# Optimization experiments

Hardware: AMD Instinct MI355X
Metric: run time of the kernel (lower is better)

## Reference

```python
import jax, jax.numpy as jnp
import numpy as np


def xnorm(x, g):
    # x * gamma / ||x||_2 along last dim (no eps, matching torch.norm)
    n = jnp.sqrt(jnp.sum(x * x, axis=-1, keepdims=True))
    return x * g / n


def setup_inputs() -> dict:
    key = jax.random.key(0)
    ks = jax.random.split(key, 6)
    B, N, D = 8, 8192, 512
    H, DK, DV = 8, 64, 64
    std = 0.001
    return {
        "queries": jax.random.normal(ks[0], (B, N, D), dtype=jnp.float32),
        # weights stored [in, out] (transposed vs torch Linear)
        "Wq": jax.random.normal(ks[1], (D, H * DK), dtype=jnp.float32) * std,
        "bq": jnp.zeros((H * DK,), dtype=jnp.float32),
        "Wk": jax.random.normal(ks[2], (D, H * DK), dtype=jnp.float32) * std,
        "bk": jnp.zeros((H * DK,), dtype=jnp.float32),
        "Wv": jax.random.normal(ks[3], (D, H * DV), dtype=jnp.float32) * std,
        "bv": jnp.zeros((H * DV,), dtype=jnp.float32),
        "Wo": jax.random.normal(ks[4], (H * DV, D), dtype=jnp.float32) * std,
        "bo": jnp.zeros((D,), dtype=jnp.float32),
        "gamma": jax.random.normal(ks[5], (1, H, 1, 1), dtype=jnp.float32),
    }


def reference(queries, Wq, bq, Wk, bk, Wv, bv, Wo, bo, gamma):
    B, N, D = queries.shape
    H, DK = 8, 64
    DV = 64
    q = (queries @ Wq + bq).reshape(B, N, H, DK)  # bnhd
    k = (queries @ Wk + bk).reshape(B, N, H, DK)
    v = (queries @ Wv + bv).reshape(B, N, H, DV)
    # kv = k^T @ v per (batch, head): [B,H,DK,DV]
    kv = jnp.einsum("bnhk,bnhv->bhkv", k, v)
    kv_n = xnorm(kv, gamma)                       # norm over DV axis
    q_n = xnorm(q.transpose(0, 2, 1, 3), gamma)   # bhnd, norm over DK axis
    out = jnp.einsum("bhnk,bhkv->bnhv", q_n, kv_n).reshape(B, N, H * DV)
    return out @ Wo + bo
```

## Files before the change

### kernel.cpp

```cpp
#include <hip/hip_runtime.h>

typedef __attribute__((ext_vector_type(8))) short s8v;
typedef __attribute__((ext_vector_type(4))) short s4v;
typedef __attribute__((ext_vector_type(4))) float f4v;

__device__ __forceinline__ unsigned short f2bf(float f) {
  unsigned int u = __float_as_uint(f);
  u += 0x7FFFu + ((u >> 16) & 1u);
  return (unsigned short)(u >> 16);
}
__device__ __forceinline__ float bf2f(unsigned short s) {
  return __uint_as_float(((unsigned int)s) << 16);
}

__device__ __forceinline__ void gld16(const void* g, void* l) {
  __builtin_amdgcn_global_load_lds(
      (const __attribute__((address_space(1))) unsigned int*)g,
      (__attribute__((address_space(3))) unsigned int*)l, 16, 0, 0);
}

#define TILE_SYNC() asm volatile("s_waitcnt vmcnt(0) lgkmcnt(0)\n\ts_barrier" ::: "memory")

__global__ __launch_bounds__(256)
void convert_x_kernel(const float* __restrict__ X, unsigned short* __restrict__ Xbf)
{
  size_t base = ((size_t)blockIdx.x * 256 + threadIdx.x) * 8;
  float4 a = *(const float4*)&X[base];
  float4 b = *(const float4*)&X[base + 4];
  s8v p = (s8v){ (short)f2bf(a.x), (short)f2bf(a.y), (short)f2bf(a.z), (short)f2bf(a.w),
                 (short)f2bf(b.x), (short)f2bf(b.y), (short)f2bf(b.z), (short)f2bf(b.w) };
  *(s8v*)&Xbf[base] = p;
}

__global__ __launch_bounds__(256)
void transpose_w_kernel(const float* __restrict__ Wq, const float* __restrict__ Wk,
                        const float* __restrict__ Wv, unsigned short* __restrict__ Wt)
{
  __shared__ float T[64][68];
  const int kt = blockIdx.x, nt = blockIdx.y;
  const float* W = (nt < 8) ? Wq : (nt < 16 ? Wk : Wv);
  const int n0 = (nt & 7) * 64, k0 = kt * 64;
  const int t = threadIdx.x;
  #pragma unroll
  for (int it = 0; it < 4; ++it) {
    int idx = it * 256 + t;
    int k = idx >> 4, n4 = (idx & 15) << 2;
    *(float4*)&T[k][n4] = *(const float4*)&W[(size_t)(k0 + k) * 512 + n0 + n4];
  }
  __syncthreads();
  #pragma unroll
  for (int it = 0; it < 2; ++it) {
    int idx = it * 256 + t;
    int n = idx >> 3, k8 = (idx & 7) << 3;
    s8v p;
    #pragma unroll
    for (int j = 0; j < 8; ++j) p[j] = (short)f2bf(T[k8 + j][n]);
    *(s8v*)&Wt[((size_t)nt * 64 + n) * 512 + k0 + k8] = p;
  }
}

__global__ __launch_bounds__(512, 2)
void gemm_qkv_kernel(const unsigned short* __restrict__ Xbf,
                     const unsigned short* __restrict__ Wt,
                     const float* __restrict__ bq, const float* __restrict__ bk,
                     const float* __restrict__ bv,
                     const float* __restrict__ gamma,
                     unsigned short* __restrict__ qkv)
{
  __shared__ short As[2][16384];
  __shared__ short Bs[2][16384];
  const int t = threadIdx.x;
  const int o = blockIdx.x;
  const int swz = (o & 7) * 192 + (o >> 3);
  const int nb = swz % 6, rb = swz / 6;
  const int wave = t >> 6, lane = t & 63;
  const int wm = wave & 1, wn = wave >> 1;
  const int quad = lane >> 4, l16 = lane & 15;
  const int row0 = rb * 256, ncol0 = nb * 256;

  const unsigned short* ap[4];
  const unsigned short* bp[4];
  int ldst[4];
  #pragma unroll
  for (int i = 0; i < 4; ++i) {
    int s = i * 512 + t;
    int m = s >> 3, kb = (s & 7) ^ (m & 7);
    ap[i] = Xbf + (size_t)(row0 + m) * 512 + kb * 8;
    bp[i] = Wt + (size_t)(ncol0 + m) * 512 + kb * 8;
    ldst[i] = s * 8;
  }

  f4v acc[8][4];
  #pragma unroll
  for (int i = 0; i < 8; ++i)
    #pragma unroll
    for (int j = 0; j < 4; ++j) acc[i][j] = (f4v){0.f, 0.f, 0.f, 0.f};

  #pragma unroll
  for (int i = 0; i < 4; ++i) {
    gld16(ap[i], &As[0][ldst[i]]);
    gld16(bp[i], &Bs[0][ldst[i]]);
  }
  TILE_SYNC();

  for (int kt = 0; kt < 8; ++kt) {
    const int cur = kt & 1;
    const short* Ac = As[cur];
    const short* Bc = Bs[cur];
    short* An = (short*)As[cur ^ 1];
    short* Bn = (short*)Bs[cur ^ 1];
    const int koff = (kt + 1) * 64;
    const bool pf = kt < 7;
    s8v afr[4][2], bfr[4][2];

    if (pf) {
      gld16(ap[0] + koff, &An[ldst[0]]);
      gld16(ap[1] + koff, &An[ldst[1]]);
      gld16(bp[0] + koff, &Bn[ldst[0]]);
      gld16(bp[1] + koff, &Bn[ldst[1]]);
    }
    #pragma unroll
    for (int nj = 0; nj < 4; ++nj)
      #pragma unroll
      for (int ks = 0; ks < 2; ++ks) {
        int r = wn * 64 + nj * 16 + l16;
        bfr[nj][ks] = *(const s8v*)&Bc[(r * 8 + ((ks * 4 + quad) ^ (r & 7))) * 8];
      }
    #pragma unroll
    for (int mi = 0; mi < 4; ++mi)
      #pragma unroll
      for (int ks = 0; ks < 2; ++ks) {
        int r = wm * 128 + mi * 16 + l16;
        afr[mi][ks] = *(const s8v*)&Ac[(r * 8 + ((ks * 4 + quad) ^ (r & 7))) * 8];
      }
    __builtin_amdgcn_s_setprio(1);
    #pragma unroll
    for (int mi = 0; mi < 4; ++mi)
      #pragma unroll
      for (int nj = 0; nj < 2; ++nj)
        #pragma unroll
        for (int ks = 0; ks < 2; ++ks)
          acc[mi][nj] = __builtin_amdgcn_mfma_f32_16x16x32_bf16(afr[mi][ks], bfr[nj][ks], acc[mi][nj], 0, 0, 0);
    __builtin_amdgcn_s_setprio(0);
    __builtin_amdgcn_s_barrier();

    if (pf) {
      gld16(ap[2] + koff, &An[ldst[2]]);
      gld16(ap[3] + koff, &An[ldst[3]]);
      gld16(bp[2] + koff, &Bn[ldst[2]]);
      gld16(bp[3] + koff, &Bn[ldst[3]]);
    }
    __builtin_amdgcn_s_setprio(1);
    #pragma unroll
    for (int mi = 0; mi < 4; ++mi)
      #pragma unroll
      for (int nj = 2; nj < 4; ++nj)
        #pragma unroll
        for (int ks = 0; ks < 2; ++ks)
          acc[mi][nj] = __builtin_amdgcn_mfma_f32_16x16x32_bf16(afr[mi][ks], bfr[nj][ks], acc[mi][nj], 0, 0, 0);
    __builtin_amdgcn_s_setprio(0);
    __builtin_amdgcn_s_barrier();

    #pragma unroll
    for (int mi = 0; mi < 4; ++mi)
      #pragma unroll
      for (int ks = 0; ks < 2; ++ks) {
        int r = wm * 128 + (4 + mi) * 16 + l16;
        afr[mi][ks] = *(const s8v*)&Ac[(r * 8 + ((ks * 4 + quad) ^ (r & 7))) * 8];
      }
    __builtin_amdgcn_s_setprio(1);
    #pragma unroll
    for (int mi = 0; mi < 4; ++mi)
      #pragma unroll
      for (int nj = 0; nj < 2; ++nj)
        #pragma unroll
        for (int ks = 0; ks < 2; ++ks)
          acc[4 + mi][nj] = __builtin_amdgcn_mfma_f32_16x16x32_bf16(afr[mi][ks], bfr[nj][ks], acc[4 + mi][nj], 0, 0, 0);
    __builtin_amdgcn_s_setprio(0);
    __builtin_amdgcn_s_barrier();

    __builtin_amdgcn_s_setprio(1);
    #pragma unroll
    for (int mi = 0; mi < 4; ++mi)
      #pragma unroll
      for (int nj = 2; nj < 4; ++nj)
        #pragma unroll
        for (int ks = 0; ks < 2; ++ks)
          acc[4 + mi][nj] = __builtin_amdgcn_mfma_f32_16x16x32_bf16(afr[mi][ks], bfr[nj][ks], acc[4 + mi][nj], 0, 0, 0);
    __builtin_amdgcn_s_setprio(0);
    TILE_SYNC();
  }

  #pragma unroll
  for (int nj = 0; nj < 4; ++nj) {
    int colg = ncol0 + wn * 64 + nj * 16 + l16;
    float bias;
    if (colg < 512) bias = bq[colg];
    else if (colg < 1024) bias = bk[colg - 512];
    else bias = bv[colg - 1024];
    #pragma unroll
    for (int mi = 0; mi < 8; ++mi) {
      acc[mi][nj][0] += bias; acc[mi][nj][1] += bias;
      acc[mi][nj][2] += bias; acc[mi][nj][3] += bias;
    }
  }

  if (nb < 2) {
    float g = gamma[nb * 4 + wn];
    #pragma unroll
    for (int mi = 0; mi < 8; ++mi)
      #pragma unroll
      for (int rr = 0; rr < 4; ++rr) {
        float ss = acc[mi][0][rr] * acc[mi][0][rr] + acc[mi][1][rr] * acc[mi][1][rr]
                 + acc[mi][2][rr] * acc[mi][2][rr] + acc[mi][3][rr] * acc[mi][3][rr];
        ss += __shfl_xor(ss, 1);
        ss += __shfl_xor(ss, 2);
        ss += __shfl_xor(ss, 4);
        ss += __shfl_xor(ss, 8);
        float scale = g * rsqrtf(ss);
        acc[mi][0][rr] *= scale; acc[mi][1][rr] *= scale;
        acc[mi][2][rr] *= scale; acc[mi][3][rr] *= scale;
      }
  }

  const int colbase = ncol0 + wn * 64;
  #pragma unroll
  for (int mi = 0; mi < 8; ++mi)
    #pragma unroll
    for (int nj = 0; nj < 4; ++nj)
      #pragma unroll
      for (int rr = 0; rr < 4; ++rr) {
        int row = row0 + wm * 128 + mi * 16 + quad * 4 + rr;
        int col = colbase + nj * 16 + l16;
        qkv[(size_t)row * 1536 + col] = f2bf(acc[mi][nj][rr]);
      }
}

__global__ __launch_bounds__(256)
void kv_accum_kernel(const unsigned short* __restrict__ qkv, float* __restrict__ kvpart)
{
  __shared__ float ksf[16][64];
  __shared__ float vsf[16][64];
  const int t = threadIdx.x;
  const int bh = blockIdx.x, chunk = blockIdx.y;
  const int b = bh >> 3, h = bh & 7;
  const int base_row = b * 8192 + chunk * 512;
  const int lane = t & 63, wave = t >> 6;
  const int dk0 = (lane & 7) * 8, dv0 = (lane >> 3) * 8;
  const int half = t >> 7, tt = t & 127;
  const int sr = tt >> 3, u = tt & 7;
  const int col = (half ? 1024 : 512) + h * 64 + u * 8;
  const unsigned short* src = qkv + (size_t)(base_row + sr) * 1536 + col;
  float* dstlds = half ? &vsf[sr][u * 8] : &ksf[sr][u * 8];
  float acc[8][8] = {};

  for (int it = 0; it < 32; ++it) {
    __syncthreads();
    union { int4 v; unsigned short s[8]; } raw;
    raw.v = *(const int4*)(src + (size_t)it * 16 * 1536);
    float4 lo = { bf2f(raw.s[0]), bf2f(raw.s[1]), bf2f(raw.s[2]), bf2f(raw.s[3]) };
    float4 hi = { bf2f(raw.s[4]), bf2f(raw.s[5]), bf2f(raw.s[6]), bf2f(raw.s[7]) };
    *(float4*)dstlds = lo;
    *(float4*)(dstlds + 4) = hi;
    __syncthreads();
    #pragma unroll
    for (int rr = 0; rr < 4; ++rr) {
      int r = rr * 4 + wave;
      float4 ka = *(const float4*)&ksf[r][dk0];
      float4 kb = *(const float4*)&ksf[r][dk0 + 4];
      float4 va = *(const float4*)&vsf[r][dv0];
      float4 vb = *(const float4*)&vsf[r][dv0 + 4];
      float kf[8] = { ka.x, ka.y, ka.z, ka.w, kb.x, kb.y, kb.z, kb.w };
      float vf[8] = { va.x, va.y, va.z, va.w, vb.x, vb.y, vb.z, vb.w };
      #pragma unroll
      for (int i = 0; i < 8; ++i)
        #pragma unroll
        for (int j = 0; j < 8; ++j)
          acc[i][j] = fmaf(kf[i], vf[j], acc[i][j]);
    }
  }
  float* dst = kvpart + ((size_t)(chunk * 4 + wave) * 64 + bh) * 4096;
  #pragma unroll
  for (int i = 0; i < 8; ++i) {
    *(float4*)&dst[(dk0 + i) * 64 + dv0]     = (float4){ acc[i][0], acc[i][1], acc[i][2], acc[i][3] };
    *(float4*)&dst[(dk0 + i) * 64 + dv0 + 4] = (float4){ acc[i][4], acc[i][5], acc[i][6], acc[i][7] };
  }
}

__global__ __launch_bounds__(256)
void kv_reduce_kernel(const float* __restrict__ kvpart, float* __restrict__ kvbuf)
{
  const int bh = blockIdx.x, seg = blockIdx.y, t = threadIdx.x;
  #pragma unroll
  for (int e = 0; e < 2; ++e) {
    int i = seg * 512 + e * 256 + t;
    float s = 0.f;
    for (int c = 0; c < 64; ++c) s += kvpart[((size_t)c * 64 + bh) * 4096 + i];
    kvbuf[(size_t)bh * 4096 + i] = s;
  }
}

__global__ __launch_bounds__(256)
void build_w2t_kernel(const float* __restrict__ kvbuf, const float* __restrict__ Wo,
                      const float* __restrict__ gamma, unsigned short* __restrict__ W2t)
{
  __shared__ float WoS[512][16];
  const int b = blockIdx.x, dt = blockIdx.y;
  const int d0 = dt * 16;
  const int t = threadIdx.x;
  for (int i = 0; i < 32; ++i) {
    int flat = i * 256 + t;
    int rr_ = flat >> 4, c = flat & 15;
    WoS[rr_][c] = Wo[(size_t)rr_ * 512 + d0 + c];
  }
  __syncthreads();
  for (int rr = 0; rr < 2; ++rr) {
    int r = rr * 256 + t;
    int h = r >> 6, k = r & 63;
    const float* krow = kvbuf + ((size_t)b * 8 + h) * 4096 + (size_t)k * 64;
    float ss = 0.f;
    #pragma unroll
    for (int v = 0; v < 64; v += 4) {
      float4 x = *(const float4*)&krow[v];
      ss += x.x * x.x + x.y * x.y + x.z * x.z + x.w * x.w;
    }
    float scale = gamma[h] * rsqrtf(ss);
    f4v accv[4];
    #pragma unroll
    for (int j = 0; j < 4; ++j) accv[j] = (f4v){0.f, 0.f, 0.f, 0.f};
    for (int v = 0; v < 64; ++v) {
      float m = krow[v] * scale;
      const float* w = &WoS[h * 64 + v][0];
      #pragma unroll
      for (int j4 = 0; j4 < 4; ++j4) {
        float4 ww = *(const float4*)&w[j4 * 4];
        accv[j4][0] = fmaf(m, ww.x, accv[j4][0]);
        accv[j4][1] = fmaf(m, ww.y, accv[j4][1]);
        accv[j4][2] = fmaf(m, ww.z, accv[j4][2]);
        accv[j4][3] = fmaf(m, ww.w, accv[j4][3]);
      }
    }
    #pragma unroll
    for (int j = 0; j < 16; ++j)
      W2t[((size_t)b * 512 + d0 + j) * 512 + r] = f2bf(accv[j >> 2][j & 3]);
  }
}

__global__ __launch_bounds__(512, 2)
void gemm_out_kernel(const unsigned short* __restrict__ qkv,
                     const unsigned short* __restrict__ W2t,
                     const float* __restrict__ bo,
                     float* __restrict__ out)
{
  __shared__ short As[2][16384];
  __shared__ short Bs[2][16384];
  const int t = threadIdx.x;
  const int o = blockIdx.x;
  const int swz = (o & 7) * 64 + (o >> 3);
  const int nb = swz & 1, rb = swz >> 1;
  const int wave = t >> 6, lane = t & 63;
  const int wm = wave & 1, wn = wave >> 1;
  const int quad = lane >> 4, l16 = lane & 15;
  const int row0 = rb * 256, ncol0 = nb * 256;
  const unsigned short* Wb = W2t + (size_t)(rb >> 5) * 262144;

  const unsigned short* ap[4];
  const unsigned short* bp[4];
  int ldst[4];
  #pragma unroll
  for (int i = 0; i < 4; ++i) {
    int s = i * 512 + t;
    int m = s >> 3, kb = (s & 7) ^ (m & 7);
    ap[i] = qkv + (size_t)(row0 + m) * 1536 + kb * 8;
    bp[i] = Wb + (size_t)(ncol0 + m) * 512 + kb * 8;
    ldst[i] = s * 8;
  }

  f4v acc[8][4];
  #pragma unroll
  for (int i = 0; i < 8; ++i)
    #pragma unroll
    for (int j = 0; j < 4; ++j) acc[i][j] = (f4v){0.f, 0.f, 0.f, 0.f};

  #pragma unroll
  for (int i = 0; i < 4; ++i) {
    gld16(ap[i], &As[0][ldst[i]]);
    gld16(bp[i], &Bs[0][ldst[i]]);
  }
  TILE_SYNC();

  for (int kt = 0; kt < 8; ++kt) {
    const int cur = kt & 1;
    const short* Ac = As[cur];
    const short* Bc = Bs[cur];
    short* An = (short*)As[cur ^ 1];
    short* Bn = (short*)Bs[cur ^ 1];
    const int koff = (kt + 1) * 64;
    const bool pf = kt < 7;
    s8v afr[4][2], bfr[4][2];

    if (pf) {
      gld16(ap[0] + koff, &An[ldst[0]]);
      gld16(ap[1] + koff, &An[ldst[1]]);
      gld16(bp[0] + koff, &Bn[ldst[0]]);
      gld16(bp[1] + koff, &Bn[ldst[1]]);
    }
    #pragma unroll
    for (int nj = 0; nj < 4; ++nj)
      #pragma unroll
      for (int ks = 0; ks < 2; ++ks) {
        int r = wn * 64 + nj * 16 + l16;
        bfr[nj][ks] = *(const s8v*)&Bc[(r * 8 + ((ks * 4 + quad) ^ (r & 7))) * 8];
      }
    #pragma unroll
    for (int mi = 0; mi < 4; ++mi)
      #pragma unroll
      for (int ks = 0; ks < 2; ++ks) {
        int r = wm * 128 + mi * 16 + l16;
        afr[mi][ks] = *(const s8v*)&Ac[(r * 8 + ((ks * 4 + quad) ^ (r & 7))) * 8];
      }
    __builtin_amdgcn_s_setprio(1);
    #pragma unroll
    for (int mi = 0; mi < 4; ++mi)
      #pragma unroll
      for (int nj = 0; nj < 2; ++nj)
        #pragma unroll
        for (int ks = 0; ks < 2; ++ks)
          acc[mi][nj] = __builtin_amdgcn_mfma_f32_16x16x32_bf16(afr[mi][ks], bfr[nj][ks], acc[mi][nj], 0, 0, 0);
    __builtin_amdgcn_s_setprio(0);
    __builtin_amdgcn_s_barrier();

    if (pf) {
      gld16(ap[2] + koff, &An[ldst[2]]);
      gld16(ap[3] + koff, &An[ldst[3]]);
      gld16(bp[2] + koff, &Bn[ldst[2]]);
      gld16(bp[3] + koff, &Bn[ldst[3]]);
    }
    __builtin_amdgcn_s_setprio(1);
    #pragma unroll
    for (int mi = 0; mi < 4; ++mi)
      #pragma unroll
      for (int nj = 2; nj < 4; ++nj)
        #pragma unroll
        for (int ks = 0; ks < 2; ++ks)
          acc[mi][nj] = __builtin_amdgcn_mfma_f32_16x16x32_bf16(afr[mi][ks], bfr[nj][ks], acc[mi][nj], 0, 0, 0);
    __builtin_amdgcn_s_setprio(0);
    __builtin_amdgcn_s_barrier();

    #pragma unroll
    for (int mi = 0; mi < 4; ++mi)
      #pragma unroll
      for (int ks = 0; ks < 2; ++ks) {
        int r = wm * 128 + (4 + mi) * 16 + l16;
        afr[mi][ks] = *(const s8v*)&Ac[(r * 8 + ((ks * 4 + quad) ^ (r & 7))) * 8];
      }
    __builtin_amdgcn_s_setprio(1);
    #pragma unroll
    for (int mi = 0; mi < 4; ++mi)
      #pragma unroll
      for (int nj = 0; nj < 2; ++nj)
        #pragma unroll
        for (int ks = 0; ks < 2; ++ks)
          acc[4 + mi][nj] = __builtin_amdgcn_mfma_f32_16x16x32_bf16(afr[mi][ks], bfr[nj][ks], acc[4 + mi][nj], 0, 0, 0);
    __builtin_amdgcn_s_setprio(0);
    __builtin_amdgcn_s_barrier();

    __builtin_amdgcn_s_setprio(1);
    #pragma unroll
    for (int mi = 0; mi < 4; ++mi)
      #pragma unroll
      for (int nj = 2; nj < 4; ++nj)
        #pragma unroll
        for (int ks = 0; ks < 2; ++ks)
          acc[4 + mi][nj] = __builtin_amdgcn_mfma_f32_16x16x32_bf16(afr[mi][ks], bfr[nj][ks], acc[4 + mi][nj], 0, 0, 0);
    __builtin_amdgcn_s_setprio(0);
    TILE_SYNC();
  }

  const int colbase = ncol0 + wn * 64;
  #pragma unroll
  for (int nj = 0; nj < 4; ++nj) {
    float bias = bo[colbase + nj * 16 + l16];
    #pragma unroll
    for (int mi = 0; mi < 8; ++mi)
      #pragma unroll
      for (int rr = 0; rr < 4; ++rr) {
        int row = row0 + wm * 128 + mi * 16 + quad * 4 + rr;
        int col = colbase + nj * 16 + l16;
        out[(size_t)row * 512 + col] = acc[mi][nj][rr] + bias;
      }
  }
}

extern "C" void kernel_launch(void* const* d_in, const int* in_sizes, int n_in,
                              void* d_out, int out_size, void* d_ws, size_t ws_size,
                              hipStream_t stream)
{
  (void)in_sizes; (void)n_in; (void)out_size; (void)ws_size;
  const float* X     = (const float*)d_in[0];
  const float* Wq    = (const float*)d_in[1];
  const float* bq    = (const float*)d_in[2];
  const float* Wk    = (const float*)d_in[3];
  const float* bk    = (const float*)d_in[4];
  const float* Wv    = (const float*)d_in[5];
  const float* bv    = (const float*)d_in[6];
  const float* Wo    = (const float*)d_in[7];
  const float* bo    = (const float*)d_in[8];
  const float* gamma = (const float*)d_in[9];

  char* ws = (char*)d_ws;
  unsigned short* qkv = (unsigned short*)ws;
  unsigned short* Xbf = (unsigned short*)(ws + 201326592);
  float* kvpart = (float*)(ws + 201326592);
  unsigned short* Wt  = (unsigned short*)(ws + 201326592 + 67108864);
  float* kvbuf        = (float*)(ws + 201326592 + 67108864 + 1572864);
  unsigned short* W2t = (unsigned short*)(ws + 201326592 + 67108864 + 1572864 + 1048576);

  dim3 blk(256);
  convert_x_kernel<<<16384, blk, 0, stream>>>(X, Xbf);
  transpose_w_kernel<<<dim3(8, 24), blk, 0, stream>>>(Wq, Wk, Wv, Wt);
  gemm_qkv_kernel<<<1536, dim3(512), 0, stream>>>(Xbf, Wt, bq, bk, bv, gamma, qkv);
  kv_accum_kernel<<<dim3(64, 16), blk, 0, stream>>>(qkv, kvpart);
  kv_reduce_kernel<<<dim3(64, 8), blk, 0, stream>>>(kvpart, kvbuf);
  build_w2t_kernel<<<dim3(8, 32), blk, 0, stream>>>(kvbuf, Wo, gamma, W2t);
  gemm_out_kernel<<<512, dim3(512), 0, stream>>>(qkv, W2t, bo, (float*)d_out);
}
```

Baseline: 530.6 us.

## Store K/V transposed from QKV GEMM and use MFMA for KV accumulation

The QKV GEMM now writes normalized Q into a compact row-major buffer and writes K and V transposed (feature-major along the sequence), so the KV accumulation can load MFMA operands directly from global memory and use bf16 matrix cores instead of scalar FMAs through LDS. The GEMM tile is shrunk from 256x256 with 512 threads, double-buffered and prioritized, to a 128x128 single-buffered loop with 256 threads. This removes the scalar FP32 outer-product cost in kv_accum and the strided reads of the wide qkv buffer. In exchange it gives up the software pipelining in the main GEMM and adds scattered transposed stores.

Result: faster. 504.8 us (-4.9%).

```diff
diff --git a/kernel.cpp b/kernel.cpp
--- a/kernel.cpp
+++ b/kernel.cpp
@@ -1,7 +1,6 @@
 #include <hip/hip_runtime.h>
 
 typedef __attribute__((ext_vector_type(8))) short s8v;
-typedef __attribute__((ext_vector_type(4))) short s4v;
 typedef __attribute__((ext_vector_type(4))) float f4v;
 
 __device__ __forceinline__ unsigned short f2bf(float f) {
@@ -59,156 +58,88 @@
   }
 }
 
-__global__ __launch_bounds__(512, 2)
+__global__ __launch_bounds__(256, 2)
 void gemm_qkv_kernel(const unsigned short* __restrict__ Xbf,
                      const unsigned short* __restrict__ Wt,
                      const float* __restrict__ bq, const float* __restrict__ bk,
                      const float* __restrict__ bv,
                      const float* __restrict__ gamma,
-                     unsigned short* __restrict__ qkv)
-{
-  __shared__ short As[2][16384];
-  __shared__ short Bs[2][16384];
+                     unsigned short* __restrict__ qhat,
+                     unsigned short* __restrict__ kvT)
+{
+  __shared__ short As[8192];
+  __shared__ short Bs[8192];
   const int t = threadIdx.x;
-  const int o = blockIdx.x;
-  const int swz = (o & 7) * 192 + (o >> 3);
-  const int nb = swz % 6, rb = swz / 6;
+  const int nb = blockIdx.x, rb = blockIdx.y;
   const int wave = t >> 6, lane = t & 63;
   const int wm = wave & 1, wn = wave >> 1;
   const int quad = lane >> 4, l16 = lane & 15;
-  const int row0 = rb * 256, ncol0 = nb * 256;
+  const int row0 = rb * 128;
+  const int ncol0 = nb * 128;
 
   const unsigned short* ap[4];
   const unsigned short* bp[4];
-  int ldst[4];
   #pragma unroll
   for (int i = 0; i < 4; ++i) {
-    int s = i * 512 + t;
-    int m = s >> 3, kb = (s & 7) ^ (m & 7);
+    int s = i * 256 + t;
+    int m = s >> 3;
+    int kb = (s & 7) ^ (m & 7);
     ap[i] = Xbf + (size_t)(row0 + m) * 512 + kb * 8;
     bp[i] = Wt + (size_t)(ncol0 + m) * 512 + kb * 8;
-    ldst[i] = s * 8;
-  }
-
-  f4v acc[8][4];
-  #pragma unroll
-  for (int i = 0; i < 8; ++i)
+  }
+
+  f4v acc[4][4];
+  #pragma unroll
+  for (int i = 0; i < 4; ++i)
     #pragma unroll
     for (int j = 0; j < 4; ++j) acc[i][j] = (f4v){0.f, 0.f, 0.f, 0.f};
 
-  #pragma unroll
-  for (int i = 0; i < 4; ++i) {
-    gld16(ap[i], &As[0][ldst[i]]);
-    gld16(bp[i], &Bs[0][ldst[i]]);
-  }
-  TILE_SYNC();
-
-  for (int kt = 0; kt < 8; ++kt) {
-    const int cur = kt & 1;
-    const short* Ac = As[cur];
-    const short* Bc = Bs[cur];
-    short* An = (short*)As[cur ^ 1];
-    short* Bn = (short*)Bs[cur ^ 1];
-    const int koff = (kt + 1) * 64;
-    const bool pf = kt < 7;
-    s8v afr[4][2], bfr[4][2];
-
-    if (pf) {
-      gld16(ap[0] + koff, &An[ldst[0]]);
-      gld16(ap[1] + koff, &An[ldst[1]]);
-      gld16(bp[0] + koff, &Bn[ldst[0]]);
-      gld16(bp[1] + koff, &Bn[ldst[1]]);
-    }
-    #pragma unroll
-    for (int nj = 0; nj < 4; ++nj)
-      #pragma unroll
-      for (int ks = 0; ks < 2; ++ks) {
+  for (int kt = 0; kt < 512; kt += 64) {
+    __syncthreads();
+    #pragma unroll
+    for (int i = 0; i < 4; ++i) {
+      int s8 = (i * 256 + t) * 8;
+      gld16(ap[i] + kt, &As[s8]);
+      gld16(bp[i] + kt, &Bs[s8]);
+    }
+    __syncthreads();
+    #pragma unroll
+    for (int ks = 0; ks < 2; ++ks) {
+      s8v a[4], b[4];
+      #pragma unroll
+      for (int mi = 0; mi < 4; ++mi) {
+        int r = wm * 64 + mi * 16 + l16;
+        int slot = r * 8 + ((ks * 4 + quad) ^ (r & 7));
+        a[mi] = *(const s8v*)&As[slot * 8];
+      }
+      #pragma unroll
+      for (int nj = 0; nj < 4; ++nj) {
         int r = wn * 64 + nj * 16 + l16;
-        bfr[nj][ks] = *(const s8v*)&Bc[(r * 8 + ((ks * 4 + quad) ^ (r & 7))) * 8];
-      }
-    #pragma unroll
-    for (int mi = 0; mi < 4; ++mi)
-      #pragma unroll
-      for (int ks = 0; ks < 2; ++ks) {
-        int r = wm * 128 + mi * 16 + l16;
-        afr[mi][ks] = *(const s8v*)&Ac[(r * 8 + ((ks * 4 + quad) ^ (r & 7))) * 8];
-      }
-    __builtin_amdgcn_s_setprio(1);
-    #pragma unroll
-    for (int mi = 0; mi < 4; ++mi)
-      #pragma unroll
-      for (int nj = 0; nj < 2; ++nj)
-        #pragma unroll
-        for (int ks = 0; ks < 2; ++ks)
-          acc[mi][nj] = __builtin_amdgcn_mfma_f32_16x16x32_bf16(afr[mi][ks], bfr[nj][ks], acc[mi][nj], 0, 0, 0);
-    __builtin_amdgcn_s_setprio(0);
-    __builtin_amdgcn_s_barrier();
-
-    if (pf) {
-      gld16(ap[2] + koff, &An[ldst[2]]);
-      gld16(ap[3] + koff, &An[ldst[3]]);
-      gld16(bp[2] + koff, &Bn[ldst[2]]);
-      gld16(bp[3] + koff, &Bn[ldst[3]]);
-    }
-    __builtin_amdgcn_s_setprio(1);
-    #pragma unroll
-    for (int mi = 0; mi < 4; ++mi)
-      #pragma unroll
-      for (int nj = 2; nj < 4; ++nj)
-        #pragma unroll
-        for (int ks = 0; ks < 2; ++ks)
-          acc[mi][nj] = __builtin_amdgcn_mfma_f32_16x16x32_bf16(afr[mi][ks], bfr[nj][ks], acc[mi][nj], 0, 0, 0);
-    __builtin_amdgcn_s_setprio(0);
-    __builtin_amdgcn_s_barrier();
-
-    #pragma unroll
-    for (int mi = 0; mi < 4; ++mi)
-      #pragma unroll
-      for (int ks = 0; ks < 2; ++ks) {
-        int r = wm * 128 + (4 + mi) * 16 + l16;
-        afr[mi][ks] = *(const s8v*)&Ac[(r * 8 + ((ks * 4 + quad) ^ (r & 7))) * 8];
-      }
-    __builtin_amdgcn_s_setprio(1);
-    #pragma unroll
-    for (int mi = 0; mi < 4; ++mi)
-      #pragma unroll
-      for (int nj = 0; nj < 2; ++nj)
-        #pragma unroll
-        for (int ks = 0; ks < 2; ++ks)
-          acc[4 + mi][nj] = __builtin_amdgcn_mfma_f32_16x16x32_bf16(afr[mi][ks], bfr[nj][ks], acc[4 + mi][nj], 0, 0, 0);
-    __builtin_amdgcn_s_setprio(0);
-    __builtin_amdgcn_s_barrier();
-
-    __builtin_amdgcn_s_setprio(1);
-    #pragma unroll
-    for (int mi = 0; mi < 4; ++mi)
-      #pragma unroll
-      for (int nj = 2; nj < 4; ++nj)
-        #pragma unroll
-        for (int ks = 0; ks < 2; ++ks)
-          acc[4 + mi][nj] = __builtin_amdgcn_mfma_f32_16x16x32_bf16(afr[mi][ks], bfr[nj][ks], acc[4 + mi][nj], 0, 0, 0);
-    __builtin_amdgcn_s_setprio(0);
-    TILE_SYNC();
-  }
-
-  #pragma unroll
-  for (int nj = 0; nj < 4; ++nj) {
-    int colg = ncol0 + wn * 64 + nj * 16 + l16;
-    float bias;
-    if (colg < 512) bias = bq[colg];
-    else if (colg < 1024) bias = bk[colg - 512];
-    else bias = bv[colg - 1024];
-    #pragma unroll
-    for (int mi = 0; mi < 8; ++mi) {
-      acc[mi][nj][0] += bias; acc[mi][nj][1] += bias;
-      acc[mi][nj][2] += bias; acc[mi][nj][3] += bias;
-    }
-  }
-
-  if (nb < 2) {
-    float g = gamma[nb * 4 + wn];
-    #pragma unroll
-    for (int mi = 0; mi < 8; ++mi)
+        int slot = r * 8 + ((ks * 4 + quad) ^ (r & 7));
+        b[nj] = *(const s8v*)&Bs[slot * 8];
+      }
+      #pragma unroll
+      for (int mi = 0; mi < 4; ++mi)
+        #pragma unroll
+        for (int nj = 0; nj < 4; ++nj)
+          acc[mi][nj] = __builtin_amdgcn_mfma_f32_16x16x32_bf16(a[mi], b[nj], acc[mi][nj], 0, 0, 0);
+    }
+  }
+
+  if (nb < 4) {
+    #pragma unroll
+    for (int nj = 0; nj < 4; ++nj) {
+      int colg = ncol0 + wn * 64 + nj * 16 + l16;
+      float bias = bq[colg];
+      #pragma unroll
+      for (int mi = 0; mi < 4; ++mi) {
+        acc[mi][nj][0] += bias; acc[mi][nj][1] += bias;
+        acc[mi][nj][2] += bias; acc[mi][nj][3] += bias;
+      }
+    }
+    float g = gamma[nb * 2 + wn];
+    #pragma unroll
+    for (int mi = 0; mi < 4; ++mi)
       #pragma unroll
       for (int rr = 0; rr < 4; ++rr) {
         float ss = acc[mi][0][rr] * acc[mi][0][rr] + acc[mi][1][rr] * acc[mi][1][rr]
@@ -221,70 +152,98 @@
         acc[mi][0][rr] *= scale; acc[mi][1][rr] *= scale;
         acc[mi][2][rr] *= scale; acc[mi][3][rr] *= scale;
       }
-  }
-
-  const int colbase = ncol0 + wn * 64;
-  #pragma unroll
-  for (int mi = 0; mi < 8; ++mi)
-    #pragma unroll
-    for (int nj = 0; nj < 4; ++nj)
-      #pragma unroll
-      for (int rr = 0; rr < 4; ++rr) {
-        int row = row0 + wm * 128 + mi * 16 + quad * 4 + rr;
-        int col = colbase + nj * 16 + l16;
-        qkv[(size_t)row * 1536 + col] = f2bf(acc[mi][nj][rr]);
-      }
+    const int colbase = ncol0 + wn * 64;
+    #pragma unroll
+    for (int mi = 0; mi < 4; ++mi)
+      #pragma unroll
+      for (int nj = 0; nj < 4; ++nj)
+        #pragma unroll
+        for (int rr = 0; rr < 4; ++rr) {
+          int row = row0 + wm * 64 + mi * 16 + quad * 4 + rr;
+          int col = colbase + nj * 16 + l16;
+          qhat[(size_t)row * 512 + col] = f2bf(acc[mi][nj][rr]);
+        }
+  } else {
+    const int sect = (nb - 4) >> 2;
+    const float* bb = sect ? bv : bk;
+    const int bidx = row0 >> 13;
+    const int nb4 = (nb - 4) & 3;
+    const int nrow = (row0 & 8191) + wm * 64 + quad * 4;
+    #pragma unroll
+    for (int nj = 0; nj < 4; ++nj) {
+      int cis = nb4 * 128 + wn * 64 + nj * 16 + l16;
+      float bias = bb[cis];
+      int h = cis >> 6, dk = cis & 63;
+      unsigned short* rowp = kvT + (size_t)((sect * 64 + bidx * 8 + h) * 64 + dk) * 8192;
+      #pragma unroll
+      for (int mi = 0; mi < 4; ++mi) {
+        unsigned int lo = (unsigned int)f2bf(acc[mi][nj][0] + bias)
+                        | ((unsigned int)f2bf(acc[mi][nj][1] + bias) << 16);
+        unsigned int hi = (unsigned int)f2bf(acc[mi][nj][2] + bias)
+                        | ((unsigned int)f2bf(acc[mi][nj][3] + bias) << 16);
+        uint2 pk; pk.x = lo; pk.y = hi;
+        *(uint2*)&rowp[nrow + mi * 16] = pk;
+      }
+    }
+  }
 }
 
 __global__ __launch_bounds__(256)
-void kv_accum_kernel(const unsigned short* __restrict__ qkv, float* __restrict__ kvpart)
-{
-  __shared__ float ksf[16][64];
-  __shared__ float vsf[16][64];
+void kv_accum_kernel(const unsigned short* __restrict__ kvT, float* __restrict__ kvpart)
+{
   const int t = threadIdx.x;
   const int bh = blockIdx.x, chunk = blockIdx.y;
-  const int b = bh >> 3, h = bh & 7;
-  const int base_row = b * 8192 + chunk * 512;
-  const int lane = t & 63, wave = t >> 6;
-  const int dk0 = (lane & 7) * 8, dv0 = (lane >> 3) * 8;
-  const int half = t >> 7, tt = t & 127;
-  const int sr = tt >> 3, u = tt & 7;
-  const int col = (half ? 1024 : 512) + h * 64 + u * 8;
-  const unsigned short* src = qkv + (size_t)(base_row + sr) * 1536 + col;
-  float* dstlds = half ? &vsf[sr][u * 8] : &ksf[sr][u * 8];
-  float acc[8][8] = {};
-
-  for (int it = 0; it < 32; ++it) {
-    __syncthreads();
-    union { int4 v; unsigned short s[8]; } raw;
-    raw.v = *(const int4*)(src + (size_t)it * 16 * 1536);
-    float4 lo = { bf2f(raw.s[0]), bf2f(raw.s[1]), bf2f(raw.s[2]), bf2f(raw.s[3]) };
-    float4 hi = { bf2f(raw.s[4]), bf2f(raw.s[5]), bf2f(raw.s[6]), bf2f(raw.s[7]) };
-    *(float4*)dstlds = lo;
-    *(float4*)(dstlds + 4) = hi;
-    __syncthreads();
-    #pragma unroll
-    for (int rr = 0; rr < 4; ++rr) {
-      int r = rr * 4 + wave;
-      float4 ka = *(const float4*)&ksf[r][dk0];
-      float4 kb = *(const float4*)&ksf[r][dk0 + 4];
-      float4 va = *(const float4*)&vsf[r][dv0];
-      float4 vb = *(const float4*)&vsf[r][dv0 + 4];
-      float kf[8] = { ka.x, ka.y, ka.z, ka.w, kb.x, kb.y, kb.z, kb.w };
-      float vf[8] = { va.x, va.y, va.z, va.w, vb.x, vb.y, vb.z, vb.w };
-      #pragma unroll
-      for (int i = 0; i < 8; ++i)
-        #pragma unroll
-        for (int j = 0; j < 8; ++j)
-          acc[i][j] = fmaf(kf[i], vf[j], acc[i][j]);
-    }
-  }
+  const int wave = t >> 6, lane = t & 63;
+  const int quad = lane >> 4, l16 = lane & 15;
+  const unsigned short* kb_ = kvT + (size_t)bh * 64 * 8192;
+  const unsigned short* vb_ = kvT + (size_t)(64 + bh) * 64 * 8192;
+  const int n0 = chunk * 512 + wave * 128 + quad * 8;
+
+  f4v acc[4][4];
+  #pragma unroll
+  for (int i = 0; i < 4; ++i)
+    #pragma unroll
+    for (int j = 0; j < 4; ++j) acc[i][j] = (f4v){0.f, 0.f, 0.f, 0.f};
+
+  s8v a0[4], b0[4], a1[4], b1[4];
+  #pragma unroll
+  for (int mi = 0; mi < 4; ++mi) {
+    a0[mi] = *(const s8v*)&kb_[(size_t)(mi * 16 + l16) * 8192 + n0];
+    b0[mi] = *(const s8v*)&vb_[(size_t)(mi * 16 + l16) * 8192 + n0];
+  }
+
+#define KV_STEP(AC, BC, AN, BN, S)                                             \
+  {                                                                            \
+    if ((S) < 3) {                                                             \
+      int nn = n0 + ((S) + 1) * 32;                                            \
+      _Pragma("unroll")                                                        \
+      for (int mi = 0; mi < 4; ++mi) {                                         \
+        AN[mi] = *(const s8v*)&kb_[(size_t)(mi * 16 + l16) * 8192 + nn];       \
+        BN[mi] = *(const s8v*)&vb_[(size_t)(mi * 16 + l16) * 8192 + nn];       \
+      }                                                                        \
+    }                                                                          \
+    _Pragma("unroll")                                                          \
+    for (int mi = 0; mi < 4; ++mi)                                             \
+      _Pragma("unroll")                                                        \
+      for (int nj = 0; nj < 4; ++nj)                                           \
+        acc[mi][nj] = __builtin_amdgcn_mfma_f32_16x16x32_bf16(AC[mi], BC[nj],  \
+                                                              acc[mi][nj], 0, 0, 0); \
+  }
+
+  KV_STEP(a0, b0, a1, b1, 0)
+  KV_STEP(a1, b1, a0, b0, 1)
+  KV_STEP(a0, b0, a1, b1, 2)
+  KV_STEP(a1, b1, a0, b0, 3)
+#undef KV_STEP
+
   float* dst = kvpart + ((size_t)(chunk * 4 + wave) * 64 + bh) * 4096;
   #pragma unroll
-  for (int i = 0; i < 8; ++i) {
-    *(float4*)&dst[(dk0 + i) * 64 + dv0]     = (float4){ acc[i][0], acc[i][1], acc[i][2], acc[i][3] };
-    *(float4*)&dst[(dk0 + i) * 64 + dv0 + 4] = (float4){ acc[i][4], acc[i][5], acc[i][6], acc[i][7] };
-  }
+  for (int mi = 0; mi < 4; ++mi)
+    #pragma unroll
+    for (int nj = 0; nj < 4; ++nj)
+      #pragma unroll
+      for (int rr = 0; rr < 4; ++rr)
+        dst[(mi * 16 + quad * 4 + rr) * 64 + nj * 16 + l16] = acc[mi][nj][rr];
 }
 
 __global__ __launch_bounds__(256)
@@ -347,7 +306,7 @@
 }
 
 __global__ __launch_bounds__(512, 2)
-void gemm_out_kernel(const unsigned short* __restrict__ qkv,
+void gemm_out_kernel(const unsigned short* __restrict__ qhat,
                      const unsigned short* __restrict__ W2t,
                      const float* __restrict__ bo,
                      float* __restrict__ out)
@@ -371,7 +330,7 @@
   for (int i = 0; i < 4; ++i) {
     int s = i * 512 + t;
     int m = s >> 3, kb = (s & 7) ^ (m & 7);
-    ap[i] = qkv + (size_t)(row0 + m) * 1536 + kb * 8;
+    ap[i] = qhat + (size_t)(row0 + m) * 512 + kb * 8;
     bp[i] = Wb + (size_t)(ncol0 + m) * 512 + kb * 8;
     ldst[i] = s * 8;
   }
@@ -509,8 +468,9 @@
   const float* gamma = (const float*)d_in[9];
 
   char* ws = (char*)d_ws;
-  unsigned short* qkv = (unsigned short*)ws;
-  unsigned short* Xbf = (unsigned short*)(ws + 201326592);
+  unsigned short* qhat = (unsigned short*)ws;
+  unsigned short* kvT  = (unsigned short*)(ws + 67108864);
+  unsigned short* Xbf  = (unsigned short*)(ws + 201326592);
   float* kvpart = (float*)(ws + 201326592);
   unsigned short* Wt  = (unsigned short*)(ws + 201326592 + 67108864);
   float* kvbuf        = (float*)(ws + 201326592 + 67108864 + 1572864);
@@ -519,9 +479,9 @@
   dim3 blk(256);
   convert_x_kernel<<<16384, blk, 0, stream>>>(X, Xbf);
   transpose_w_kernel<<<dim3(8, 24), blk, 0, stream>>>(Wq, Wk, Wv, Wt);
-  gemm_qkv_kernel<<<1536, dim3(512), 0, stream>>>(Xbf, Wt, bq, bk, bv, gamma, qkv);
-  kv_accum_kernel<<<dim3(64, 16), blk, 0, stream>>>(qkv, kvpart);
+  gemm_qkv_kernel<<<dim3(12, 512), blk, 0, stream>>>(Xbf, Wt, bq, bk, bv, gamma, qhat, kvT);
+  kv_accum_kernel<<<dim3(64, 16), blk, 0, stream>>>(kvT, kvpart);
   kv_reduce_kernel<<<dim3(64, 8), blk, 0, stream>>>(kvpart, kvbuf);
   build_w2t_kernel<<<dim3(8, 32), blk, 0, stream>>>(kvbuf, Wo, gamma, W2t);
-  gemm_out_kernel<<<512, dim3(512), 0, stream>>>(qkv, W2t, bo, (float*)d_out);
-}
+  gemm_out_kernel<<<512, dim3(512), 0, stream>>>(qhat, W2t, bo, (float*)d_out);
+}
```
